# Kernel tuning notes

Measured on AMD Instinct MI355X. Metric: run time of the kernel, lower is better.

## Reference

```python
import jax, jax.numpy as jnp
import numpy as np

D_MODEL = 512
WINDOW = 128
N_HEADS = 8


def setup_inputs() -> dict:
    key = jax.random.key(0)
    k1, k2, k3, k4, k5 = jax.random.split(key, 5)
    B, S, D = 8, 4096, D_MODEL
    scale = 1.0 / np.sqrt(D)
    return {
        "x": jax.random.normal(k1, (B, S, D), dtype=jnp.float32),
        "in_proj_w": jax.random.normal(k2, (3 * D, D), dtype=jnp.float32) * scale,
        "in_proj_b": jax.random.normal(k3, (3 * D,), dtype=jnp.float32) * 0.02,
        "out_proj_w": jax.random.normal(k4, (D, D), dtype=jnp.float32) * scale,
        "out_proj_b": jax.random.normal(k5, (D,), dtype=jnp.float32) * 0.02,
    }


def reference(x, in_proj_w, in_proj_b, out_proj_w, out_proj_b):
    # Non-overlapping sliding-window MHA with shared weights per window.
    B, S, D = x.shape
    W = WINDOW
    H = N_HEADS
    hd = D // H
    nw = S // W  # S chosen divisible by window size

    xw = x.reshape(B, nw, W, D)
    # Fused QKV projection (torch in_proj_weight layout: [3D, D], y = x @ W^T + b)
    qkv = jnp.einsum("bnwd,ed->bnwe", xw, in_proj_w) + in_proj_b  # [B,nw,W,3D]
    q, k, v = jnp.split(qkv, 3, axis=-1)

    def to_heads(t):
        return t.reshape(B, nw, W, H, hd)

    q = to_heads(q) * (1.0 / np.sqrt(hd))
    k = to_heads(k)
    v = to_heads(v)

    # Block-diagonal attention: scores only within each window [B,nw,H,W,W]
    scores = jnp.einsum("bnqhd,bnkhd->bnhqk", q, k)
    attn = jax.nn.softmax(scores, axis=-1)
    ctx = jnp.einsum("bnhqk,bnkhd->bnqhd", attn, v)  # [B,nw,W,H,hd]
    ctx = ctx.reshape(B, S, D)

    out = jnp.einsum("bsd,ed->bse", ctx, out_proj_w) + out_proj_b
    return out
```

## Files before the change

### kernel.cpp

```cpp
#include <hip/hip_runtime.h>


typedef __bf16 bf16x8 __attribute__((ext_vector_type(8)));
typedef __bf16 bf16x4 __attribute__((ext_vector_type(4)));
typedef float  f32x4  __attribute__((ext_vector_type(4)));

#define MFMA16(a, b, c) __builtin_amdgcn_mfma_f32_16x16x32_bf16((a), (b), (c), 0, 0, 0)
#define VMCNT_(n) asm volatile("s_waitcnt vmcnt(" #n ")" ::: "memory")
#define VMCNT(n) VMCNT_(n)
#define LGKM0() asm volatile("s_waitcnt lgkmcnt(0)" ::: "memory")
#define BAR() __builtin_amdgcn_s_barrier()

__device__ __forceinline__ void gload_lds16(const __bf16* g, void* l) {
    __builtin_amdgcn_global_load_lds(
        (const __attribute__((address_space(1))) unsigned int*)g,
        (__attribute__((address_space(3))) unsigned int*)l, 16, 0, 0);
}

__device__ __forceinline__ void cvt8(const float* __restrict__ s,
                                     __bf16* __restrict__ d, long i) {
    const float4* s4 = reinterpret_cast<const float4*>(s);
    float4 a = s4[2 * i], b = s4[2 * i + 1];
    bf16x8 v;
    v[0] = (__bf16)a.x; v[1] = (__bf16)a.y; v[2] = (__bf16)a.z; v[3] = (__bf16)a.w;
    v[4] = (__bf16)b.x; v[5] = (__bf16)b.y; v[6] = (__bf16)b.z; v[7] = (__bf16)b.w;
    *reinterpret_cast<bf16x8*>(d + 8 * i) = v;
}

__global__ void convert_k(const float* __restrict__ x,
                          const float* __restrict__ w_in,
                          const float* __restrict__ w_out,
                          __bf16* __restrict__ x_bf,
                          __bf16* __restrict__ w_in_bf,
                          __bf16* __restrict__ w_out_bf)
{
    long i0 = (long)blockIdx.x * blockDim.x + threadIdx.x;
    long stride = (long)gridDim.x * blockDim.x;
    for (long i = i0; i < 16777216 / 8; i += stride) cvt8(x, x_bf, i);
    for (long i = i0; i < 786432 / 8;   i += stride) cvt8(w_in, w_in_bf, i);
    for (long i = i0; i < 262144 / 8;   i += stride) cvt8(w_out, w_out_bf, i);
}

template<int EPI, int NN>
__global__ __launch_bounds__(256, 2)
void gemmT(const __bf16* __restrict__ A,
           const __bf16* __restrict__ Bw,
           const float* __restrict__ bias,
           void* __restrict__ Cq,
           __bf16* __restrict__ vT)
{
    __shared__ __align__(16) char smem[73728];

    const int nwg = gridDim.x;
    const int chunk = nwg >> 3;
    const int bid = blockIdx.x;
    const int wg = (bid & 7) * chunk + (bid >> 3);
    const int nidx = wg % NN;
    const int midx = wg / NN;
    const long mbase = (long)midx * 256;
    const int colbase = nidx * 128;

    const int tid = threadIdx.x;
    const int w = tid >> 6, lane = tid & 63;
    const int lrow = lane & 15, hi = lane >> 4;
    const int wm = w >> 1, wn = w & 1;

    const int srow = tid >> 2;
    const int kchunk = (tid & 3) ^ ((srow >> 1) & 3);
    const __bf16* PA = A  + (mbase + srow) * 512 + kchunk * 8;
    const __bf16* PB = Bw + ((long)colbase + srow) * 512 + kchunk * 8;
    const int rd16 = (hi ^ ((lrow >> 1) & 3)) << 4;

    auto stage = [&](int t, int slot) {
        char* Ab = smem + slot * 24576;
        char* Bb = Ab + 16384;
        const int ko = t * 32;
        #pragma unroll
        for (int j = 0; j < 4; ++j)
            gload_lds16(PA + (64 * j) * 512 + ko, Ab + j * 4096 + w * 1024);
        #pragma unroll
        for (int j = 0; j < 2; ++j)
            gload_lds16(PB + (64 * j) * 512 + ko, Bb + j * 4096 + w * 1024);
    };

    f32x4 acc[8][4];
    #pragma unroll
    for (int rt = 0; rt < 8; ++rt)
        #pragma unroll
        for (int ct = 0; ct < 4; ++ct) acc[rt][ct] = (f32x4){0.f, 0.f, 0.f, 0.f};

    stage(0, 0); stage(1, 1);

    int cs = 0;
    int ss = 2;
    #pragma unroll 1
    for (int t = 0; t < 16; ++t) {
        if (t < 15) { VMCNT(6); } else { VMCNT(0); }
        LGKM0();
        BAR();
        if (t < 14) stage(t + 2, ss);
        const char* Ab = smem + cs * 24576;
        const char* Bb = Ab + 16384;
        bf16x8 af[4], bfr[4];
        #pragma unroll
        for (int ct = 0; ct < 4; ++ct)
            bfr[ct] = *reinterpret_cast<const bf16x8*>(
                Bb + (64 * wn + 16 * ct + lrow) * 64 + rd16);
        #pragma unroll
        for (int i = 0; i < 4; ++i)
            af[i] = *reinterpret_cast<const bf16x8*>(
                Ab + (128 * wm + 16 * i + lrow) * 64 + rd16);
        __builtin_amdgcn_s_setprio(1);
        #pragma unroll
        for (int i = 0; i < 4; ++i)
            #pragma unroll
            for (int ct = 0; ct < 4; ++ct)
                acc[i][ct] = MFMA16(af[i], bfr[ct], acc[i][ct]);
        __builtin_amdgcn_s_setprio(0);
        #pragma unroll
        for (int i = 0; i < 4; ++i)
            af[i] = *reinterpret_cast<const bf16x8*>(
                Ab + (128 * wm + 64 + 16 * i + lrow) * 64 + rd16);
        __builtin_amdgcn_s_setprio(1);
        #pragma unroll
        for (int i = 0; i < 4; ++i)
            #pragma unroll
            for (int ct = 0; ct < 4; ++ct)
                acc[4 + i][ct] = MFMA16(af[i], bfr[ct], acc[4 + i][ct]);
        __builtin_amdgcn_s_setprio(0);
        cs = (cs == 2) ? 0 : cs + 1;
        ss = (ss == 2) ? 0 : ss + 1;
    }
    LGKM0();
    BAR();

    if (EPI == 0) {
        if (colbase < 1024) {
            const float scale = (colbase < 512) ? 0.125f : 1.0f;
            __bf16* qk = (__bf16*)Cq;
            #pragma unroll
            for (int ct = 0; ct < 4; ++ct) {
                int col = 64 * wn + 16 * ct + lrow;
                float b = bias[colbase + col];
                #pragma unroll
                for (int rt = 0; rt < 8; ++rt)
                    #pragma unroll
                    for (int r = 0; r < 4; ++r) {
                        int row = 128 * wm + 16 * rt + 4 * hi + r;
                        *reinterpret_cast<__bf16*>(
                            smem + row * 256 + ((col * 2) ^ ((row & 15) << 4))) =
                            (__bf16)((acc[rt][ct][r] + b) * scale);
                    }
            }
            LGKM0();
            BAR();
            #pragma unroll
            for (int i = 0; i < 16; ++i) {
                int row = 16 * i + (tid >> 4);
                int slot = (tid & 15) ^ (tid >> 4);
                bf16x8 v = *reinterpret_cast<const bf16x8*>(smem + row * 256 + slot * 16);
                *reinterpret_cast<bf16x8*>(
                    qk + (mbase + row) * 1024 + colbase + (tid & 15) * 8) = v;
            }
        } else {
            #pragma unroll
            for (int ct = 0; ct < 4; ++ct) {
                int e = 64 * wn + 16 * ct + lrow;
                float b = bias[colbase + e];
                #pragma unroll
                for (int rt = 0; rt < 8; ++rt) {
                    int tok0 = 128 * wm + 16 * rt + 4 * hi;
                    bf16x4 pk;
                    pk[0] = (__bf16)(acc[rt][ct][0] + b);
                    pk[1] = (__bf16)(acc[rt][ct][1] + b);
                    pk[2] = (__bf16)(acc[rt][ct][2] + b);
                    pk[3] = (__bf16)(acc[rt][ct][3] + b);
                    *reinterpret_cast<bf16x4*>(
                        smem + e * 512 + ((tok0 * 2) ^ ((e & 15) << 4))) = pk;
                }
            }
            LGKM0();
            BAR();
            #pragma unroll
            for (int i = 0; i < 16; ++i) {
                int e = 8 * i + (tid >> 5);
                int gch = tid & 31;
                int slot = gch ^ (e & 15);
                bf16x8 v = *reinterpret_cast<const bf16x8*>(smem + e * 512 + slot * 16);
                long win = 2 * midx + (gch >> 4);
                *reinterpret_cast<bf16x8*>(
                    vT + (win * 512 + (colbase - 1024 + e)) * 128 + (gch & 15) * 8) = v;
            }
        }
    } else {
        float* outp = (float*)Cq;
        #pragma unroll
        for (int ct = 0; ct < 4; ++ct) {
            int colg = colbase + 64 * wn + 16 * ct + lrow;
            float b = bias[colg];
            #pragma unroll
            for (int rt = 0; rt < 8; ++rt) {
                long row = mbase + 128 * wm + 16 * rt + 4 * hi;
                #pragma unroll
                for (int r = 0; r < 4; ++r)
                    outp[(row + r) * 512 + colg] = acc[rt][ct][r] + b;
            }
        }
    }
}

__global__ __launch_bounds__(256)
void swa_attn(const __bf16* __restrict__ qk,
              const __bf16* __restrict__ vT,
              __bf16* __restrict__ ctx)
{
    __shared__ __bf16 p_lds[4][32][136];

    const int bid = blockIdx.x;
    const int win = bid >> 3, h = bid & 7;
    const int tid = threadIdx.x;
    const int w = tid >> 6, lane = tid & 63;
    const int lrow = lane & 15, hi = lane >> 4;
    const long tokb = (long)win * 128;

    bf16x8 qa[2][2];
    #pragma unroll
    for (int rt = 0; rt < 2; ++rt)
        #pragma unroll
        for (int ks = 0; ks < 2; ++ks)
            qa[rt][ks] = *reinterpret_cast<const bf16x8*>(
                qk + (tokb + 32 * w + 16 * rt + lrow) * 1024 + h * 64 + ks * 32 + hi * 8);

    f32x4 s[2][8];
    #pragma unroll
    for (int rt = 0; rt < 2; ++rt)
        #pragma unroll
        for (int ct = 0; ct < 8; ++ct) s[rt][ct] = (f32x4){0.f, 0.f, 0.f, 0.f};
    #pragma unroll
    for (int ks = 0; ks < 2; ++ks) {
        #pragma unroll
        for (int ct = 0; ct < 8; ++ct) {
            bf16x8 kb = *reinterpret_cast<const bf16x8*>(
                qk + (tokb + 16 * ct + lrow) * 1024 + 512 + h * 64 + ks * 32 + hi * 8);
            s[0][ct] = MFMA16(qa[0][ks], kb, s[0][ct]);
            s[1][ct] = MFMA16(qa[1][ks], kb, s[1][ct]);
        }
    }

    float inv[2][4];
    #pragma unroll
    for (int rt = 0; rt < 2; ++rt) {
        #pragma unroll
        for (int r = 0; r < 4; ++r) {
            float m = s[rt][0][r];
            #pragma unroll
            for (int ct = 1; ct < 8; ++ct) m = fmaxf(m, s[rt][ct][r]);
            m = fmaxf(m, __shfl_xor(m, 1));
            m = fmaxf(m, __shfl_xor(m, 2));
            m = fmaxf(m, __shfl_xor(m, 4));
            m = fmaxf(m, __shfl_xor(m, 8));
            float sum = 0.f;
            #pragma unroll
            for (int ct = 0; ct < 8; ++ct) {
                float e = __expf(s[rt][ct][r] - m);
                sum += e;
                p_lds[w][16 * rt + 4 * hi + r][16 * ct + lrow] = (__bf16)e;
            }
            sum += __shfl_xor(sum, 1);
            sum += __shfl_xor(sum, 2);
            sum += __shfl_xor(sum, 4);
            sum += __shfl_xor(sum, 8);
            inv[rt][r] = 1.f / sum;
        }
    }

    f32x4 o[2][4];
    #pragma unroll
    for (int rt = 0; rt < 2; ++rt)
        #pragma unroll
        for (int ct = 0; ct < 4; ++ct) o[rt][ct] = (f32x4){0.f, 0.f, 0.f, 0.f};
    const __bf16* vb = vT + (long)win * 512 * 128 + (long)h * 64 * 128;
    #pragma unroll
    for (int kt = 0; kt < 4; ++kt) {
        bf16x8 pa0 = *reinterpret_cast<const bf16x8*>(&p_lds[w][lrow][32 * kt + 8 * hi]);
        bf16x8 pa1 = *reinterpret_cast<const bf16x8*>(&p_lds[w][16 + lrow][32 * kt + 8 * hi]);
        #pragma unroll
        for (int ct = 0; ct < 4; ++ct) {
            bf16x8 vf = *reinterpret_cast<const bf16x8*>(
                vb + (16 * ct + lrow) * 128 + 32 * kt + 8 * hi);
            o[0][ct] = MFMA16(pa0, vf, o[0][ct]);
            o[1][ct] = MFMA16(pa1, vf, o[1][ct]);
        }
    }

    #pragma unroll
    for (int rt = 0; rt < 2; ++rt)
        #pragma unroll
        for (int ct = 0; ct < 4; ++ct)
            #pragma unroll
            for (int r = 0; r < 4; ++r) {
                long tok = tokb + 32 * w + 16 * rt + 4 * hi + r;
                ctx[tok * 512 + h * 64 + 16 * ct + lrow] =
                    (__bf16)(o[rt][ct][r] * inv[rt][r]);
            }
}

extern "C" void kernel_launch(void* const* d_in, const int* in_sizes, int n_in,
                              void* d_out, int out_size, void* d_ws, size_t ws_size,
                              hipStream_t stream)
{
    const float* x     = (const float*)d_in[0];
    const float* w_in  = (const float*)d_in[1];
    const float* b_in  = (const float*)d_in[2];
    const float* w_out = (const float*)d_in[3];
    const float* b_out = (const float*)d_in[4];

    char* ws = (char*)d_ws;
    __bf16* x_bf     = (__bf16*)(ws);
    __bf16* ctx      = (__bf16*)(ws);
    __bf16* vT       = (__bf16*)(ws + 33554432);
    __bf16* w_in_bf  = (__bf16*)(ws + 67108864);
    __bf16* w_out_bf = (__bf16*)(ws + 68681728);
    __bf16* qk       = (__bf16*)d_out;

    convert_k<<<2048, 256, 0, stream>>>(x, w_in, w_out, x_bf, w_in_bf, w_out_bf);
    gemmT<0, 12><<<1536, 256, 0, stream>>>(x_bf, w_in_bf, b_in, (void*)qk, vT);
    swa_attn<<<2048, 256, 0, stream>>>(qk, vT, ctx);
    gemmT<1, 4><<<512, 256, 0, stream>>>(ctx, w_out_bf, b_out, d_out, nullptr);
}
```

Measured before the change: 160.0 us.

## Use 256x256 GEMM tiles with 512 threads and a 5-slot K-interleaved LDS ring

Rewrites the projection GEMM so each 512-thread workgroup computes a 256x256 output tile, halving the number of workgroups. K is streamed in 16-element chunks through a five-slot LDS ring, using a plane-split layout in place of the XOR swizzle, and two chunks are consumed per barrier. The epilogue is staged through LDS in two passes because of the larger tile. The attention kernel also remaps block IDs across XCDs. Together these aim to cut global and LDS traffic per FLOP, at the cost of fewer workgroups and more epilogue barriers.

```diff
diff --git a/kernel.cpp b/kernel.cpp
--- a/kernel.cpp
+++ b/kernel.cpp
@@ -42,74 +42,77 @@
 }
 
 template<int EPI, int NN>
-__global__ __launch_bounds__(256, 2)
-void gemmT(const __bf16* __restrict__ A,
+__global__ __launch_bounds__(512, 2)
+void gemm2(const __bf16* __restrict__ A,
            const __bf16* __restrict__ Bw,
            const float* __restrict__ bias,
            void* __restrict__ Cq,
            __bf16* __restrict__ vT)
 {
-    __shared__ __align__(16) char smem[73728];
+    __shared__ __align__(16) char smem[81920];
 
     const int nwg = gridDim.x;
-    const int chunk = nwg >> 3;
+    const int chunkx = nwg >> 3;
     const int bid = blockIdx.x;
-    const int wg = (bid & 7) * chunk + (bid >> 3);
+    const int wg = (bid & 7) * chunkx + (bid >> 3);
     const int nidx = wg % NN;
     const int midx = wg / NN;
     const long mbase = (long)midx * 256;
-    const int colbase = nidx * 128;
+    const int colbase = nidx * 256;
 
     const int tid = threadIdx.x;
     const int w = tid >> 6, lane = tid & 63;
     const int lrow = lane & 15, hi = lane >> 4;
-    const int wm = w >> 1, wn = w & 1;
-
-    const int srow = tid >> 2;
-    const int kchunk = (tid & 3) ^ ((srow >> 1) & 3);
-    const __bf16* PA = A  + (mbase + srow) * 512 + kchunk * 8;
-    const __bf16* PB = Bw + ((long)colbase + srow) * 512 + kchunk * 8;
-    const int rd16 = (hi ^ ((lrow >> 1) & 3)) << 4;
-
-    auto stage = [&](int t, int slot) {
-        char* Ab = smem + slot * 24576;
-        char* Bb = Ab + 16384;
-        const int ko = t * 32;
-        #pragma unroll
-        for (int j = 0; j < 4; ++j)
-            gload_lds16(PA + (64 * j) * 512 + ko, Ab + j * 4096 + w * 1024);
-        #pragma unroll
-        for (int j = 0; j < 2; ++j)
-            gload_lds16(PB + (64 * j) * 512 + ko, Bb + j * 4096 + w * 1024);
+    const int wm = w >> 2, wn = w & 3;
+
+    const int wp = w & 1, wr = w >> 1;
+    const __bf16* PA = A  + (mbase + 64 * wr + lane) * 512 + wp * 8;
+    const __bf16* PB = Bw + ((long)colbase + 64 * wr + lane) * 512 + wp * 8;
+    const int aoff = wp * 4096 + wr * 1024;
+
+    auto stage = [&](int c, int slot) {
+        char* sb = smem + slot * 16384;
+        gload_lds16(PA + c * 16, sb + aoff);
+        gload_lds16(PB + c * 16, sb + 8192 + aoff);
     };
 
+    const int hs = hi >> 1;
+    const int pl = (hi & 1) * 4096;
+
     f32x4 acc[8][4];
     #pragma unroll
     for (int rt = 0; rt < 8; ++rt)
         #pragma unroll
         for (int ct = 0; ct < 4; ++ct) acc[rt][ct] = (f32x4){0.f, 0.f, 0.f, 0.f};
 
-    stage(0, 0); stage(1, 1);
-
-    int cs = 0;
-    int ss = 2;
+    stage(0, 0); stage(1, 1); stage(2, 2);
+    VMCNT(2);
+    BAR();
+
+    int s0 = 0;
     #pragma unroll 1
-    for (int t = 0; t < 16; ++t) {
-        if (t < 15) { VMCNT(6); } else { VMCNT(0); }
-        LGKM0();
-        BAR();
-        if (t < 14) stage(t + 2, ss);
-        const char* Ab = smem + cs * 24576;
-        const char* Bb = Ab + 16384;
+    for (int j = 0; j < 16; ++j) {
+        if (j) {
+            if (j == 15) { VMCNT(0); } else { VMCNT(2); }
+            LGKM0();
+            BAR();
+        }
+        int t3 = s0 + 3; if (t3 >= 5) t3 -= 5;
+        int t4 = s0 + 4; if (t4 >= 5) t4 -= 5;
+        if (2 * j + 3 <= 31) stage(2 * j + 3, t3);
+        if (2 * j + 4 <= 31) stage(2 * j + 4, t4);
+        int s1 = s0 + 1; if (s1 >= 5) s1 -= 5;
+        const char* base0 = smem + s0 * 16384;
+        const char* base1 = smem + s1 * 16384;
+        const char* Ab = (hs ? base1 : base0) + pl;
+        const char* Bb = Ab + 8192;
         bf16x8 af[4], bfr[4];
         #pragma unroll
         for (int ct = 0; ct < 4; ++ct)
-            bfr[ct] = *reinterpret_cast<const bf16x8*>(
-                Bb + (64 * wn + 16 * ct + lrow) * 64 + rd16);
+            bfr[ct] = *reinterpret_cast<const bf16x8*>(Bb + (64 * wn + 16 * ct + lrow) * 16);
         #pragma unroll
         for (int i = 0; i < 4; ++i)
-            af[i] = *reinterpret_cast<const bf16x8*>(
-                Ab + (128 * wm + 16 * i + lrow) * 64 + rd16);
+            af[i] = *reinterpret_cast<const bf16x8*>(Ab + (128 * wm + 16 * i + lrow) * 16);
         __builtin_amdgcn_s_setprio(1);
         #pragma unroll
         for (int i = 0; i < 4; ++i)
@@ -119,8 +122,7 @@
         __builtin_amdgcn_s_setprio(0);
         #pragma unroll
         for (int i = 0; i < 4; ++i)
-            af[i] = *reinterpret_cast<const bf16x8*>(
-                Ab + (128 * wm + 64 + 16 * i + lrow) * 64 + rd16);
+            af[i] = *reinterpret_cast<const bf16x8*>(Ab + (128 * wm + 64 + 16 * i + lrow) * 16);
         __builtin_amdgcn_s_setprio(1);
         #pragma unroll
         for (int i = 0; i < 4; ++i)
@@ -128,8 +130,7 @@
             for (int ct = 0; ct < 4; ++ct)
                 acc[4 + i][ct] = MFMA16(af[i], bfr[ct], acc[4 + i][ct]);
         __builtin_amdgcn_s_setprio(0);
-        cs = (cs == 2) ? 0 : cs + 1;
-        ss = (ss == 2) ? 0 : ss + 1;
+        s0 += 2; if (s0 >= 5) s0 -= 5;
     }
     LGKM0();
     BAR();
@@ -138,58 +139,72 @@
         if (colbase < 1024) {
             const float scale = (colbase < 512) ? 0.125f : 1.0f;
             __bf16* qk = (__bf16*)Cq;
-            #pragma unroll
-            for (int ct = 0; ct < 4; ++ct) {
-                int col = 64 * wn + 16 * ct + lrow;
-                float b = bias[colbase + col];
+            #pragma unroll 1
+            for (int p = 0; p < 2; ++p) {
+                if (wm == p) {
+                    #pragma unroll
+                    for (int ct = 0; ct < 4; ++ct) {
+                        int col = 64 * wn + 16 * ct + lrow;
+                        float b = bias[colbase + col];
+                        #pragma unroll
+                        for (int rt = 0; rt < 8; ++rt)
+                            #pragma unroll
+                            for (int r = 0; r < 4; ++r) {
+                                int row = 16 * rt + 4 * hi + r;
+                                *reinterpret_cast<__bf16*>(
+                                    smem + row * 512 + ((col * 2) ^ ((row & 31) << 4))) =
+                                    (__bf16)((acc[rt][ct][r] + b) * scale);
+                            }
+                    }
+                }
+                LGKM0();
+                BAR();
                 #pragma unroll
-                for (int rt = 0; rt < 8; ++rt)
+                for (int i = 0; i < 8; ++i) {
+                    int row = 16 * i + (tid >> 5);
+                    int ch = tid & 31;
+                    int slot = ch ^ (row & 31);
+                    bf16x8 v = *reinterpret_cast<const bf16x8*>(smem + row * 512 + slot * 16);
+                    *reinterpret_cast<bf16x8*>(
+                        qk + (mbase + 128 * p + row) * 1024 + colbase + ch * 8) = v;
+                }
+                BAR();
+            }
+        } else {
+            #pragma unroll 1
+            for (int p = 0; p < 2; ++p) {
+                if ((wn >> 1) == p) {
                     #pragma unroll
-                    for (int r = 0; r < 4; ++r) {
-                        int row = 128 * wm + 16 * rt + 4 * hi + r;
-                        *reinterpret_cast<__bf16*>(
-                            smem + row * 256 + ((col * 2) ^ ((row & 15) << 4))) =
-                            (__bf16)((acc[rt][ct][r] + b) * scale);
+                    for (int ct = 0; ct < 4; ++ct) {
+                        int e_row = 64 * (wn & 1) + 16 * ct + lrow;
+                        float b = bias[colbase + 128 * p + e_row];
+                        #pragma unroll
+                        for (int rt = 0; rt < 8; ++rt) {
+                            int tok = 128 * wm + 16 * rt + 4 * hi;
+                            bf16x4 pk;
+                            pk[0] = (__bf16)(acc[rt][ct][0] + b);
+                            pk[1] = (__bf16)(acc[rt][ct][1] + b);
+                            pk[2] = (__bf16)(acc[rt][ct][2] + b);
+                            pk[3] = (__bf16)(acc[rt][ct][3] + b);
+                            *reinterpret_cast<bf16x4*>(
+                                smem + e_row * 512 + ((tok * 2) ^ ((e_row & 15) << 4))) = pk;
+                        }
                     }
-            }
-            LGKM0();
-            BAR();
-            #pragma unroll
-            for (int i = 0; i < 16; ++i) {
-                int row = 16 * i + (tid >> 4);
-                int slot = (tid & 15) ^ (tid >> 4);
-                bf16x8 v = *reinterpret_cast<const bf16x8*>(smem + row * 256 + slot * 16);
-                *reinterpret_cast<bf16x8*>(
-                    qk + (mbase + row) * 1024 + colbase + (tid & 15) * 8) = v;
-            }
-        } else {
-            #pragma unroll
-            for (int ct = 0; ct < 4; ++ct) {
-                int e = 64 * wn + 16 * ct + lrow;
-                float b = bias[colbase + e];
+                }
+                LGKM0();
+                BAR();
                 #pragma unroll
-                for (int rt = 0; rt < 8; ++rt) {
-                    int tok0 = 128 * wm + 16 * rt + 4 * hi;
-                    bf16x4 pk;
-                    pk[0] = (__bf16)(acc[rt][ct][0] + b);
-                    pk[1] = (__bf16)(acc[rt][ct][1] + b);
-                    pk[2] = (__bf16)(acc[rt][ct][2] + b);
-                    pk[3] = (__bf16)(acc[rt][ct][3] + b);
-                    *reinterpret_cast<bf16x4*>(
-                        smem + e * 512 + ((tok0 * 2) ^ ((e & 15) << 4))) = pk;
+                for (int i = 0; i < 8; ++i) {
+                    int e_l = 16 * i + (tid >> 5);
+                    int ch = tid & 31;
+                    int slot = ch ^ (e_l & 15);
+                    bf16x8 v = *reinterpret_cast<const bf16x8*>(smem + e_l * 512 + slot * 16);
+                    long win = 2 * midx + (ch >> 4);
+                    int eg = colbase - 1024 + 128 * p + e_l;
+                    *reinterpret_cast<bf16x8*>(
+                        vT + (win * 512 + eg) * 128 + (ch & 15) * 8) = v;
                 }
-            }
-            LGKM0();
-            BAR();
-            #pragma unroll
-            for (int i = 0; i < 16; ++i) {
-                int e = 8 * i + (tid >> 5);
-                int gch = tid & 31;
-                int slot = gch ^ (e & 15);
-                bf16x8 v = *reinterpret_cast<const bf16x8*>(smem + e * 512 + slot * 16);
-                long win = 2 * midx + (gch >> 4);
-                *reinterpret_cast<bf16x8*>(
-                    vT + (win * 512 + (colbase - 1024 + e)) * 128 + (gch & 15) * 8) = v;
+                BAR();
             }
         }
     } else {
@@ -217,7 +232,8 @@
     __shared__ __bf16 p_lds[4][32][136];
 
     const int bid = blockIdx.x;
-    const int win = bid >> 3, h = bid & 7;
+    const int wg = (bid & 7) * 256 + (bid >> 3);
+    const int win = wg >> 3, h = wg & 7;
     const int tid = threadIdx.x;
     const int w = tid >> 6, lane = tid & 63;
     const int lrow = lane & 15, hi = lane >> 4;
@@ -324,7 +340,7 @@
     __bf16* qk       = (__bf16*)d_out;
 
     convert_k<<<2048, 256, 0, stream>>>(x, w_in, w_out, x_bf, w_in_bf, w_out_bf);
-    gemmT<0, 12><<<1536, 256, 0, stream>>>(x_bf, w_in_bf, b_in, (void*)qk, vT);
+    gemm2<0, 6><<<768, 512, 0, stream>>>(x_bf, w_in_bf, b_in, (void*)qk, vT);
     swa_attn<<<2048, 256, 0, stream>>>(qk, vT, ctx);
-    gemmT<1, 4><<<512, 256, 0, stream>>>(ctx, w_out_bf, b_out, d_out, nullptr);
-}
+    gemm2<1, 2><<<256, 512, 0, stream>>>(ctx, w_out_bf, b_out, d_out, nullptr);
+}
```

Result: slower. 277.0 us (+73.1%).
